# Optimization experiments

Hardware: AMD Instinct MI355X
Metric: run time of the kernel (lower is better)

The kernel has to match this reference:

```python
import jax, jax.numpy as jnp
import numpy as np

T_STEPS, BATCH, DX, DH = 128, 128, 1024, 1024
N_GATES = 5


def setup_inputs() -> dict:
    key = jax.random.key(0)
    ks = jax.random.split(key, 4)
    scale_x = 1.0 / np.sqrt(DX)
    scale_h = 1.0 / np.sqrt(DH)
    inputs = jax.random.normal(ks[0], (T_STEPS, BATCH, DX), dtype=jnp.float32)
    memories = jax.random.normal(ks[1], (T_STEPS, BATCH, DH), dtype=jnp.float32)
    h0 = jnp.zeros((BATCH, DH), dtype=jnp.float32)
    c0 = jnp.zeros((BATCH, DH), dtype=jnp.float32)
    Wx = jax.random.normal(ks[2], (N_GATES * DH, DX), dtype=jnp.float32) * scale_x
    bx = jnp.zeros((N_GATES * DH,), dtype=jnp.float32)
    Wh = jax.random.normal(ks[3], (N_GATES * DH, DH), dtype=jnp.float32) * scale_h
    # forget-gate bias (second chunk) initialized to 1, as in reset_parameters_
    bh = jnp.zeros((N_GATES * DH,), dtype=jnp.float32).at[DH:2 * DH].set(1.0)
    return {"inputs": inputs, "memories": memories, "h0": h0, "c0": c0,
            "Wx": Wx, "bx": bx, "Wh": Wh, "bh": bh}


def reference(inputs, memories, h0, c0, Wx, bx, Wh, bh):
    # EpLSTMCell.loop: time-major scan of the custom gated cell.
    # Gate order: I, F, G, O, R (tied forget gate: it = 1 - ft).
    def step(carry, inp):
        h, c = carry
        xt, mt = inp
        gx = jnp.dot(xt, Wx.T) + bx      # [B, 5*Dh]
        gh = jnp.dot(h, Wh.T) + bh       # [B, 5*Dh]
        Xi, Xf, Xg, Xo, Xr = jnp.split(gx, N_GATES, axis=-1)
        Hi, Hf, Hg, Ho, Hr = jnp.split(gh, N_GATES, axis=-1)
        ft = jax.nn.sigmoid(Xf + Hf)
        ot = jax.nn.sigmoid(Xo + Ho)
        it = 1.0 - ft                    # tied forget gate
        gt = jnp.tanh(Xg + Hg)
        rt = jax.nn.sigmoid(Xr + Hr)     # episodic memory gate
        ct = ft * c + it * gt + rt * jnp.tanh(mt)
        ht = ot * jnp.tanh(ct)
        return (ht, ct), ht

    (_, _), outs = jax.lax.scan(step, (h0, c0), (inputs, memories))
    return outs  # [T, B, Dh]
```

## Files before the change

### kernel.cpp

```cpp
#include <hip/hip_runtime.h>

#define T_STEPS 128
#define BATCH   128
#define DX      1024
#define DH      1024
#define BDH     (BATCH * DH)
#define BDX     (BATCH * DX)
#define PLW     40

typedef __attribute__((ext_vector_type(8)))  short short8;
typedef __attribute__((ext_vector_type(16))) float f32x16;
typedef __attribute__((ext_vector_type(4)))  float f32x4v;
typedef __attribute__((ext_vector_type(2)))  float f32x2;
typedef __attribute__((ext_vector_type(4)))  unsigned u32x4;
typedef __attribute__((ext_vector_type(2)))  _Float16 f16x2;

static __device__ __forceinline__ unsigned short f2bf(float f) {
    union { float f; unsigned u; } v; v.f = f;
    unsigned r = v.u + 0x7fffu + ((v.u >> 16) & 1u);
    return (unsigned short)(r >> 16);
}
static __device__ __forceinline__ short8 pack_bf16x8(f32x4v lo, f32x4v hi) {
    union { unsigned short u[8]; short8 v; } pk;
    pk.u[0]=f2bf(lo[0]); pk.u[1]=f2bf(lo[1]); pk.u[2]=f2bf(lo[2]); pk.u[3]=f2bf(lo[3]);
    pk.u[4]=f2bf(hi[0]); pk.u[5]=f2bf(hi[1]); pk.u[6]=f2bf(hi[2]); pk.u[7]=f2bf(hi[3]);
    return pk.v;
}
static __device__ __forceinline__ float sigf(float x) {
    float u = __expf(-fabsf(x));
    float b = 1.0f / (1.0f + u);
    return x >= 0.0f ? b : 1.0f - b;
}
static __device__ __forceinline__ float tanhfast(float x) {
    float u = __expf(-2.0f * fabsf(x));
    float r = (1.0f - u) / (1.0f + u);
    return x >= 0.0f ? r : -r;
}


__global__ __launch_bounds__(256) void prep_x(const float* __restrict__ x,
                                              unsigned short* __restrict__ Xb) {
    const size_t i8 = ((size_t)blockIdx.x * 256 + threadIdx.x) * 8;
    f32x4v lo = __builtin_nontemporal_load((const f32x4v*)(x + i8));
    f32x4v hi = __builtin_nontemporal_load((const f32x4v*)(x + i8 + 4));
    short8 v = pack_bf16x8(lo, hi);
    __builtin_nontemporal_store(v, (short8*)(Xb + i8));
}

__global__ __launch_bounds__(256) void prep_tm(const float* __restrict__ mem,
                                               _Float16* __restrict__ TM) {
    const size_t i8 = ((size_t)blockIdx.x * 256 + threadIdx.x) * 8;
    f32x4v lo = __builtin_nontemporal_load((const f32x4v*)(mem + i8));
    f32x4v hi = __builtin_nontemporal_load((const f32x4v*)(mem + i8 + 4));
    union { _Float16 h[8]; u32x4 q; } V;
    #pragma unroll
    for (int j = 0; j < 4; ++j) V.h[j]     = (_Float16)tanhfast(lo[j]);
    #pragma unroll
    for (int j = 0; j < 4; ++j) V.h[4 + j] = (_Float16)tanhfast(hi[j]);
    __builtin_nontemporal_store(V.q, (u32x4*)(TM + i8));
}

__global__ __launch_bounds__(256) void init_seed(const float* __restrict__ h0,
                                                 unsigned short* __restrict__ hseq,
                                                 unsigned* __restrict__ gflag) {
    const int i = blockIdx.x * 256 + threadIdx.x;
    if (i < BDH) hseq[i] = f2bf(h0[i]);
    if (blockIdx.x < 2) gflag[blockIdx.x * 256 + threadIdx.x] = 0;
}

__global__ __launch_bounds__(128) void prep_wxp(const float* __restrict__ Wx,
                                                const float* __restrict__ bx,
                                                const float* __restrict__ bh,
                                                unsigned short* __restrict__ Wxp,
                                                float* __restrict__ bp) {
    const int p = blockIdx.x;
    const int js = p >> 5, g = (p >> 3) & 3, jj = p & 7;
    const int srow = (g + 1) * 1024 + js * 8 + jj;
    const int k = threadIdx.x * 8;
    f32x4v lo = __builtin_nontemporal_load((const f32x4v*)(Wx + (size_t)srow * DX + k));
    f32x4v hi = __builtin_nontemporal_load((const f32x4v*)(Wx + (size_t)srow * DX + k + 4));
    short8 v = pack_bf16x8(lo, hi);
    __builtin_nontemporal_store(v, (short8*)(Wxp + (size_t)p * 1024 + k));
    if (threadIdx.x == 0) bp[p] = bx[srow] + bh[srow];
}

template<bool XBF16>
__global__ __launch_bounds__(256, 2) void gx_prepass3(
    const void* __restrict__ xsrc, const unsigned short* __restrict__ Wxp,
    const float* __restrict__ bp, _Float16* __restrict__ Gx)
{
    extern __shared__ char sm[];
    _Float16* pl16 = (_Float16*)(sm + 65536);

    const int bid = blockIdx.x;
    const int c  = bid & 7;
    const int js = bid >> 3;
    const int tid = threadIdx.x;

    {
        const int row = tid >> 3;
        const int koff = (tid & 7) * 128;
        const int sw = (row & 7) << 4;
        const unsigned short* src = Wxp + (size_t)(js * 32 + row) * 1024 + koff;
        char* dst = sm + row * 2048;
        #pragma unroll
        for (int it = 0; it < 16; ++it) {
            short8 v = __builtin_nontemporal_load((const short8*)(src + it * 8));
            *(short8*)(dst + (((koff + it * 8) * 2) ^ sw)) = v;
        }
    }

    const int rrow = tid >> 1;
    const int jjb  = (tid & 1) * 4;
    float bias_f[16];
    #pragma unroll
    for (int q = 0; q < 4; ++q)
        #pragma unroll
        for (int g = 0; g < 4; ++g)
            bias_f[q * 4 + g] = bp[js * 32 + g * 8 + (jjb + q)];

    const int wave = tid >> 6, lane = tid & 63;
    const int k8 = (lane >> 5) * 8;
    const char* wrow = sm + (lane & 31) * 2048;
    const int sw2 = ((lane & 31) & 7) << 4;
    __syncthreads();

    for (int i = 0; i < 16; ++i) {
        const int mt = c * 16 + i;
        const int arow = mt * 128 + wave * 32 + (lane & 31);
        f32x16 a0 = {}, a1 = {};

        if (XBF16) {
            const unsigned short* xp = (const unsigned short*)xsrc + (size_t)arow * 1024 + k8;
            #pragma unroll 8
            for (int ks = 0; ks < 64; ++ks) {
                short8 a = *(const short8*)(xp + ks * 16);
                short8 b = *(const short8*)(wrow + ((ks * 32 + k8 * 2) ^ sw2));
                if (ks & 1) a1 = __builtin_amdgcn_mfma_f32_32x32x16_bf16(a, b, a1, 0, 0, 0);
                else        a0 = __builtin_amdgcn_mfma_f32_32x32x16_bf16(a, b, a0, 0, 0, 0);
            }
        } else {
            const float* Af = (const float*)xsrc + (size_t)arow * 1024 + k8;
            #pragma unroll 8
            for (int ks = 0; ks < 64; ++ks) {
                f32x4v lo = *(const f32x4v*)(Af + ks * 16);
                f32x4v hi = *(const f32x4v*)(Af + ks * 16 + 4);
                union { unsigned u32[4]; short8 v; } pk;
                pk.u32[0] = __builtin_amdgcn_perm(__float_as_uint(lo[1]), __float_as_uint(lo[0]), 0x07060302u);
                pk.u32[1] = __builtin_amdgcn_perm(__float_as_uint(lo[3]), __float_as_uint(lo[2]), 0x07060302u);
                pk.u32[2] = __builtin_amdgcn_perm(__float_as_uint(hi[1]), __float_as_uint(hi[0]), 0x07060302u);
                pk.u32[3] = __builtin_amdgcn_perm(__float_as_uint(hi[3]), __float_as_uint(hi[2]), 0x07060302u);
                short8 b = *(const short8*)(wrow + ((ks * 32 + k8 * 2) ^ sw2));
                if (ks & 1) a1 = __builtin_amdgcn_mfma_f32_32x32x16_bf16(pk.v, b, a1, 0, 0, 0);
                else        a0 = __builtin_amdgcn_mfma_f32_32x32x16_bf16(pk.v, b, a0, 0, 0, 0);
            }
        }
        f32x16 r = a0 + a1;

        #pragma unroll
        for (int ii = 0; ii < 16; ++ii) {
            const int rowc = (ii & 3) + 8 * (ii >> 2) + 4 * (lane >> 5);
            pl16[(wave * 32 + rowc) * 40 + (lane & 31)] = (_Float16)r[ii];
        }
        __syncthreads();

        {
            union { _Float16 h[16]; u32x4 q[2]; } V;
            #pragma unroll
            for (int q = 0; q < 4; ++q)
                #pragma unroll
                for (int g = 0; g < 4; ++g)
                    V.h[q * 4 + g] = (_Float16)(
                        (float)pl16[rrow * 40 + g * 8 + (jjb + q)] + bias_f[q * 4 + g]);
            _Float16* dst = Gx + ((size_t)(mt * 128 + rrow) * 4096 + js * 32 + jjb * 4);
            __builtin_nontemporal_store(V.q[0], (u32x4*)dst);
            __builtin_nontemporal_store(V.q[1], (u32x4*)(dst + 8));
        }
        __syncthreads();
    }
}

template<bool USE_TM>
__global__ __launch_bounds__(256, 1) void eplstm_h(
    const _Float16* __restrict__ Gx,  const void* __restrict__ tmv,
    const float* __restrict__ Wh,     const float* __restrict__ c0,
    unsigned short* __restrict__ hseq, float* __restrict__ out,
    unsigned* __restrict__ gflag)
{
    __shared__ float pl[4 * 32 * PLW];

    const int bid = blockIdx.x;
    const int js  = (bid >> 3) * 4 + (bid & 3);
    const int bhh = (bid >> 2) & 1;
    const int tid = threadIdx.x;

    const int wave = tid >> 6, lane = tid & 63;
    const int mh = wave >> 1, kh = wave & 1;
    const int arow = bhh * 64 + mh * 32 + (lane & 31);
    const int k8 = (lane >> 5) * 8;
    const int p = lane & 31;
    const int word = (p & 7) * 4 + (p >> 3);
    float* plw = pl + wave * 32 * PLW;
    unsigned long long* fb = (unsigned long long*)(gflag + bhh * 128);

    short8 breg[32];
    {
        const int r = lane & 31;
        const int g = r >> 3, jj = r & 7;
        const float* Wrow = Wh + (size_t)((g + 1) * 1024 + js * 8 + jj) * 1024
                          + kh * 512 + k8;
        #pragma unroll
        for (int ks = 0; ks < 32; ++ks) {
            f32x4v lo = *(const f32x4v*)(Wrow + ks * 16);
            f32x4v hi = *(const f32x4v*)(Wrow + ks * 16 + 4);
            breg[ks] = pack_bf16x8(lo, hi);
        }
    }

    const int e0 = tid * 2;
    const int row_e = e0 >> 3;
    const int jj0 = e0 & 7;
    const int brow = bhh * 64 + row_e;
    const size_t obase = (size_t)brow * DH + js * 8 + jj0;
    const int mh_e = row_e >> 5, r_e = row_e & 31;
    float2 creg = *(const float2*)(c0 + obase);

    for (int t = 0; t < T_STEPS; ++t) {
        u32x4 gxv = __builtin_nontemporal_load(
            (const u32x4*)(Gx + ((size_t)(t * BATCH + brow) * 4096 + js * 32 + jj0 * 4)));
        f16x2 tm2 = {};
        f32x2 mv = {};
        if (USE_TM) {
            tm2 = __builtin_nontemporal_load(
                (const f16x2*)((const _Float16*)tmv + (size_t)t * BDH + obase));
        } else {
            mv = __builtin_nontemporal_load(
                (const f32x2*)((const float*)tmv + (size_t)t * BDH + obase));
        }

        if (t > 0) {
            if (wave == 0) {
                for (;;) {
                    unsigned long long fv = __hip_atomic_load(
                        &fb[lane], __ATOMIC_RELAXED, __HIP_MEMORY_SCOPE_AGENT);
                    if (__all(((unsigned)fv >= (unsigned)t) &&
                              ((unsigned)(fv >> 32) >= (unsigned)t))) break;
                    __builtin_amdgcn_s_sleep(2);
                }
            }
            __syncthreads();
        }

        const unsigned short* hp = hseq + (size_t)t * BDH + (size_t)arow * DH + kh * 512 + k8;
        f32x16 a0 = {}, a1 = {};
        #pragma unroll
        for (int ks = 0; ks < 32; ++ks) {
            short8 a = *(const short8*)(hp + ks * 16);
            if (ks & 1) a1 = __builtin_amdgcn_mfma_f32_32x32x16_bf16(a, breg[ks], a1, 0, 0, 0);
            else        a0 = __builtin_amdgcn_mfma_f32_32x32x16_bf16(a, breg[ks], a0, 0, 0, 0);
        }
        f32x16 r = a0 + a1;
        #pragma unroll
        for (int ii = 0; ii < 16; ++ii) {
            const int rowc = (ii & 3) + 8 * (ii >> 2) + 4 * (lane >> 5);
            plw[rowc * PLW + word] = r[ii];
        }
        __syncthreads();

        float4 p0A = *(const float4*)(pl + ((((mh_e << 1) | 0) * 32 + r_e) * PLW + (jj0 + 0) * 4));
        float4 p0B = *(const float4*)(pl + ((((mh_e << 1) | 1) * 32 + r_e) * PLW + (jj0 + 0) * 4));
        float4 p1A = *(const float4*)(pl + ((((mh_e << 1) | 0) * 32 + r_e) * PLW + (jj0 + 1) * 4));
        float4 p1B = *(const float4*)(pl + ((((mh_e << 1) | 1) * 32 + r_e) * PLW + (jj0 + 1) * 4));
        union { u32x4 u; _Float16 h[8]; } G; G.u = gxv;

        float hv[2];
        {
            const float gF = (float)G.h[0] + p0A.x + p0B.x;
            const float gG = (float)G.h[1] + p0A.y + p0B.y;
            const float gO = (float)G.h[2] + p0A.z + p0B.z;
            const float gR = (float)G.h[3] + p0A.w + p0B.w;
            const float ft = sigf(gF), ot = sigf(gO), rt = sigf(gR);
            const float gt = tanhfast(gG);
            const float tmv0 = USE_TM ? (float)tm2[0] : tanhfast(mv[0]);
            const float cv = ft * creg.x + (1.f - ft) * gt + rt * tmv0;
            creg.x = cv;
            hv[0] = ot * tanhfast(cv);
        }
        {
            const float gF = (float)G.h[4] + p1A.x + p1B.x;
            const float gG = (float)G.h[5] + p1A.y + p1B.y;
            const float gO = (float)G.h[6] + p1A.z + p1B.z;
            const float gR = (float)G.h[7] + p1A.w + p1B.w;
            const float ft = sigf(gF), ot = sigf(gO), rt = sigf(gR);
            const float gt = tanhfast(gG);
            const float tmv1 = USE_TM ? (float)tm2[1] : tanhfast(mv[1]);
            const float cv = ft * creg.y + (1.f - ft) * gt + rt * tmv1;
            creg.y = cv;
            hv[1] = ot * tanhfast(cv);
        }
        const unsigned hp2 = (unsigned)f2bf(hv[0]) | ((unsigned)f2bf(hv[1]) << 16);
        __hip_atomic_store((unsigned*)(hseq + (size_t)(t + 1) * BDH + obase), hp2,
                           __ATOMIC_RELAXED, __HIP_MEMORY_SCOPE_AGENT);
        asm volatile("s_waitcnt vmcnt(0)" ::: "memory");
        __syncthreads();
        if (tid == 0 && t < T_STEPS - 1) {
            __hip_atomic_store(&gflag[bhh * 128 + js], (unsigned)(t + 1),
                               __ATOMIC_RELAXED, __HIP_MEMORY_SCOPE_AGENT);
        }
        f32x2 hvv = { hv[0], hv[1] };
        __builtin_nontemporal_store(hvv, (f32x2*)(out + (size_t)t * BDH + obase));
    }
}

template<bool XBF16>
__global__ __launch_bounds__(256, 1) void eplstm_persistent(
    const void*  __restrict__ xsrc, const float* __restrict__ mem,
    const float* __restrict__ Wx,   const float* __restrict__ Wh,
    const float* __restrict__ bxp,  const float* __restrict__ bhp,
    const float* __restrict__ c0,
    unsigned short* __restrict__ hseq, float* __restrict__ out,
    unsigned* __restrict__ bar)
{
    extern __shared__ char smem[];
    float* pl = reinterpret_cast<float*>(smem + 131072);

    const int bid = blockIdx.x;
    const int js  = bid >> 1;
    const int bhh = bid & 1;
    const int tid = threadIdx.x;

    {
        const int prow = tid >> 3;
        const int g = prow >> 3, jj = prow & 7;
        const int srow = (g + 1) * 1024 + js * 8 + jj;
        const int kc = (tid & 7) * 256;
        const int sw = (prow & 7) << 4;
        for (int it = 0; it < 32; ++it) {
            const int k = kc + it * 8;
            const float* src = (k < DX) ? (Wx + (size_t)srow * DX + k)
                                        : (Wh + (size_t)srow * DH + (k - DX));
            f32x4v lo = *(const f32x4v*)(src);
            f32x4v hi = *(const f32x4v*)(src + 4);
            short8 v = pack_bf16x8(lo, hi);
            *reinterpret_cast<short8*>(smem + prow * 4096 + ((k * 2) ^ sw)) = v;
        }
    }

    const int e0   = tid * 2;
    const int bl   = e0 >> 3;
    const int jj0  = e0 & 7;
    const int brow_g = bhh * 64 + bl;
    const size_t oidx = (size_t)brow_g * DH + js * 8 + jj0;
    float biasv[2][4];
    #pragma unroll
    for (int e2 = 0; e2 < 2; ++e2)
        #pragma unroll
        for (int g = 0; g < 4; ++g) {
            const int srow = (g + 1) * 1024 + js * 8 + jj0 + e2;
            biasv[e2][g] = bxp[srow] + bhp[srow];
        }
    float2 creg = *reinterpret_cast<const float2*>(c0 + oidx);
    const int mh_e = bl >> 5, rr = bl & 31;

    const int wave = tid >> 6;
    const int lane = tid & 63;
    const int mh = wave >> 1, kh = wave & 1;
    const int arow   = bhh * 64 + mh * 32 + (lane & 31);
    const int k8     = (lane >> 5) * 8;
    const int brow   = lane & 31;
    const char* bbase = smem + brow * 4096;
    const int swz    = (brow & 7) << 4;
    const int kbyte0 = kh * 2048 + k8 * 2;

    __syncthreads();

    for (int t = 0; t < T_STEPS; ++t) {
        f32x16 ac0 = {}, ac1 = {}, ac2 = {}, ac3 = {};
        if (XBF16 || kh == 1) {
            const unsigned short* Ab = kh
                ? (hseq + (size_t)t * BDH + (size_t)arow * DH + k8)
                : ((const unsigned short*)xsrc + (size_t)t * BDX + (size_t)arow * DX + k8);
            #pragma unroll 8
            for (int ks = 0; ks < 64; ++ks) {
                short8 a = *reinterpret_cast<const short8*>(Ab + ks * 16);
                short8 b = *reinterpret_cast<const short8*>(bbase + ((kbyte0 + ks * 32) ^ swz));
                if      ((ks & 3) == 0) ac0 = __builtin_amdgcn_mfma_f32_32x32x16_bf16(a, b, ac0, 0, 0, 0);
                else if ((ks & 3) == 1) ac1 = __builtin_amdgcn_mfma_f32_32x32x16_bf16(a, b, ac1, 0, 0, 0);
                else if ((ks & 3) == 2) ac2 = __builtin_amdgcn_mfma_f32_32x32x16_bf16(a, b, ac2, 0, 0, 0);
                else                    ac3 = __builtin_amdgcn_mfma_f32_32x32x16_bf16(a, b, ac3, 0, 0, 0);
            }
        } else {
            const float* Af = (const float*)xsrc + (size_t)t * BDX + (size_t)arow * DX + k8;
            #pragma unroll 4
            for (int ks = 0; ks < 64; ++ks) {
                f32x4v lo = *(const f32x4v*)(Af + ks * 16);
                f32x4v hi = *(const f32x4v*)(Af + ks * 16 + 4);
                short8 a = pack_bf16x8(lo, hi);
                short8 b = *reinterpret_cast<const short8*>(bbase + ((kbyte0 + ks * 32) ^ swz));
                if      ((ks & 3) == 0) ac0 = __builtin_amdgcn_mfma_f32_32x32x16_bf16(a, b, ac0, 0, 0, 0);
                else if ((ks & 3) == 1) ac1 = __builtin_amdgcn_mfma_f32_32x32x16_bf16(a, b, ac1, 0, 0, 0);
                else if ((ks & 3) == 2) ac2 = __builtin_amdgcn_mfma_f32_32x32x16_bf16(a, b, ac2, 0, 0, 0);
                else                    ac3 = __builtin_amdgcn_mfma_f32_32x32x16_bf16(a, b, ac3, 0, 0, 0);
            }
        }
        f32x16 r = (ac0 + ac1) + (ac2 + ac3);

        #pragma unroll
        for (int i = 0; i < 16; ++i) {
            const int row = (i & 3) + 8 * (i >> 2) + 4 * (lane >> 5);
            pl[(wave * 32 + row) * 33 + brow] = r[i];
        }
        __syncthreads();

        const float2 mt2 = *reinterpret_cast<const float2*>(mem + (size_t)t * BDH + oidx);
        float hv[2];
        #pragma unroll
        for (int e2 = 0; e2 < 2; ++e2) {
            const int jj = jj0 + e2;
            float gs[4];
            #pragma unroll
            for (int g = 0; g < 4; ++g) {
                const int col = g * 8 + jj;
                gs[g] = pl[((mh_e * 2 + 0) * 32 + rr) * 33 + col]
                      + pl[((mh_e * 2 + 1) * 32 + rr) * 33 + col]
                      + biasv[e2][g];
            }
            const float ft = 1.f / (1.f + expf(-gs[0]));
            const float gt = tanhf(gs[1]);
            const float ot = 1.f / (1.f + expf(-gs[2]));
            const float rt = 1.f / (1.f + expf(-gs[3]));
            const float cin = e2 ? creg.y : creg.x;
            const float mvv = e2 ? mt2.y : mt2.x;
            const float cv = ft * cin + (1.f - ft) * gt + rt * tanhf(mvv);
            if (e2) creg.y = cv; else creg.x = cv;
            hv[e2] = ot * tanhf(cv);
        }
        *reinterpret_cast<float2*>(out + (size_t)t * BDH + oidx) = make_float2(hv[0], hv[1]);
        const unsigned hpk = (unsigned)f2bf(hv[0]) | ((unsigned)f2bf(hv[1]) << 16);
        __hip_atomic_store((unsigned*)(hseq + (size_t)(t + 1) * BDH + oidx), hpk,
                           __ATOMIC_RELAXED, __HIP_MEMORY_SCOPE_AGENT);

        __syncthreads();
        if (t < T_STEPS - 1) {
            if (tid == 0) {
                const unsigned want = (unsigned)(t + 1);
                const unsigned arrived = __hip_atomic_fetch_add(
                    &bar[bhh * 32], 1u, __ATOMIC_RELAXED, __HIP_MEMORY_SCOPE_AGENT);
                if (arrived == want * 128u - 1u) {
                    __hip_atomic_store(&bar[64 + bhh * 32], want,
                                       __ATOMIC_RELAXED, __HIP_MEMORY_SCOPE_AGENT);
                } else {
                    while (__hip_atomic_load(&bar[64 + bhh * 32],
                                             __ATOMIC_RELAXED, __HIP_MEMORY_SCOPE_AGENT) < want)
                        __builtin_amdgcn_s_sleep(2);
                }
            }
            __syncthreads();
        }
    }
}

extern "C" void kernel_launch(void* const* d_in, const int* in_sizes, int n_in,
                              void* d_out, int out_size, void* d_ws, size_t ws_size,
                              hipStream_t stream) {
    const float* inputs   = (const float*)d_in[0];
    const float* memories = (const float*)d_in[1];
    const float* h0       = (const float*)d_in[2];
    const float* c0       = (const float*)d_in[3];
    const float* Wx       = (const float*)d_in[4];
    const float* bx       = (const float*)d_in[5];
    const float* Wh       = (const float*)d_in[6];
    const float* bh_      = (const float*)d_in[7];
    float* outp = (float*)d_out;

    char* ws = (char*)d_ws;
    size_t off = 0;
    auto alloc = [&](size_t bytes) {
        char* p = ws + off;
        off = (off + bytes + 255) & ~(size_t)255;
        return p;
    };
    unsigned*       gflag = (unsigned*)alloc(512 * sizeof(unsigned));
    unsigned short* hseq  = (unsigned short*)alloc((size_t)(T_STEPS + 1) * BDH * 2);

    const size_t wxp_b  = (size_t)4096 * 1024 * 2;
    const size_t bp_b   = 4096 * 4;
    const size_t gx_b   = (size_t)16384 * 4096 * 2;
    const size_t xb_b   = (size_t)T_STEPS * BDX * 2;
    const size_t tm_b   = (size_t)T_STEPS * BDH * 2;
    const size_t need_base = off + wxp_b + 256 + bp_b + 256 + gx_b + 256;
    const size_t need_xb   = need_base + xb_b + 256;
    const size_t need_tm   = need_xb + tm_b + 256;

    if (ws_size >= need_base) {
        unsigned short* Wxp = (unsigned short*)alloc(wxp_b);
        float*          bp  = (float*)alloc(bp_b);
        _Float16*       Gx  = (_Float16*)alloc(gx_b);
        const bool use_xb = (ws_size >= need_xb);
        unsigned short* Xb = use_xb ? (unsigned short*)alloc(xb_b) : nullptr;
        const bool use_tm = (ws_size >= need_tm);
        _Float16* TM = use_tm ? (_Float16*)alloc(tm_b) : nullptr;

        init_seed<<<512, 256, 0, stream>>>(h0, hseq, gflag);
        prep_wxp<<<4096, 128, 0, stream>>>(Wx, bx, bh_, Wxp, bp);
        if (use_tm) prep_tm<<<8192, 256, 0, stream>>>(memories, TM);

        const unsigned pre_smem = 65536 + 128 * 40 * 2;
        if (use_xb) {
            prep_x<<<8192, 256, 0, stream>>>(inputs, Xb);
            (void)hipFuncSetAttribute((const void*)gx_prepass3<true>,
                                      hipFuncAttributeMaxDynamicSharedMemorySize, pre_smem);
            gx_prepass3<true><<<1024, 256, pre_smem, stream>>>((const void*)Xb, Wxp, bp, Gx);
        } else {
            (void)hipFuncSetAttribute((const void*)gx_prepass3<false>,
                                      hipFuncAttributeMaxDynamicSharedMemorySize, pre_smem);
            gx_prepass3<false><<<1024, 256, pre_smem, stream>>>((const void*)inputs, Wxp, bp, Gx);
        }

        const void* tmv = use_tm ? (const void*)TM : (const void*)memories;
        if (use_tm) {
            void* kargs[] = { (void*)&Gx, (void*)&tmv, (void*)&Wh, (void*)&c0,
                              (void*)&hseq, (void*)&outp, (void*)&gflag };
            hipError_t err = hipLaunchCooperativeKernel((const void*)eplstm_h<true>,
                                                        dim3(256), dim3(256), kargs, 0, stream);
            if (err != hipSuccess)
                eplstm_h<true><<<256, 256, 0, stream>>>(Gx, tmv, Wh, c0, hseq, outp, gflag);
        } else {
            void* kargs[] = { (void*)&Gx, (void*)&tmv, (void*)&Wh, (void*)&c0,
                              (void*)&hseq, (void*)&outp, (void*)&gflag };
            hipError_t err = hipLaunchCooperativeKernel((const void*)eplstm_h<false>,
                                                        dim3(256), dim3(256), kargs, 0, stream);
            if (err != hipSuccess)
                eplstm_h<false><<<256, 256, 0, stream>>>(Gx, tmv, Wh, c0, hseq, outp, gflag);
        }
    } else {
        const bool use_xb = (ws_size >= off + xb_b + 256);
        unsigned short* Xb = use_xb ? (unsigned short*)alloc(xb_b) : nullptr;

        init_seed<<<512, 256, 0, stream>>>(h0, hseq, gflag);
        if (use_xb) prep_x<<<8192, 256, 0, stream>>>(inputs, Xb);

        const unsigned smem_bytes = 131072 + 9216 + 9216 + 64;
        const void* xsrc = use_xb ? (const void*)Xb : (const void*)inputs;
        if (use_xb) {
            (void)hipFuncSetAttribute((const void*)eplstm_persistent<true>,
                                      hipFuncAttributeMaxDynamicSharedMemorySize, smem_bytes);
            void* kargs[] = { (void*)&xsrc, (void*)&memories, (void*)&Wx, (void*)&Wh,
                              (void*)&bx, (void*)&bh_, (void*)&c0, (void*)&hseq,
                              (void*)&outp, (void*)&gflag };
            hipError_t err = hipLaunchCooperativeKernel(
                (const void*)eplstm_persistent<true>, dim3(256), dim3(256),
                kargs, smem_bytes, stream);
            if (err != hipSuccess) {
                eplstm_persistent<true><<<256, 256, smem_bytes, stream>>>(
                    xsrc, memories, Wx, Wh, bx, bh_, c0, hseq, outp, gflag);
            }
        } else {
            (void)hipFuncSetAttribute((const void*)eplstm_persistent<false>,
                                      hipFuncAttributeMaxDynamicSharedMemorySize, smem_bytes);
            void* kargs[] = { (void*)&xsrc, (void*)&memories, (void*)&Wx, (void*)&Wh,
                              (void*)&bx, (void*)&bh_, (void*)&c0, (void*)&hseq,
                              (void*)&outp, (void*)&gflag };
            hipError_t err = hipLaunchCooperativeKernel(
                (const void*)eplstm_persistent<false>, dim3(256), dim3(256),
                kargs, smem_bytes, stream);
            if (err != hipSuccess) {
                eplstm_persistent<false><<<256, 256, smem_bytes, stream>>>(
                    xsrc, memories, Wx, Wh, bx, bh_, c0, hseq, outp, gflag);
            }
        }
    }
}
```

Baseline: 1.625 ms.

## Fuse input projection into persistent recurrent kernel, computing it two steps ahead

Drops the separate Gx prepass kernel and the large fp16 Gx buffer. The recurrent cooperative kernel now keeps a bf16 slice of Wx in LDS and computes the input-gate MFMA for step t+2 after finishing step t, double-buffered in shared memory. The aim is to hide the x projection under the latency-bound serial recurrence and avoid writing and re-reading the Gx tensor. In exchange it adds per-step MFMA work and LDS pressure to the critical-path kernel, which could lengthen each step.

```diff
diff --git a/kernel.cpp b/kernel.cpp
--- a/kernel.cpp
+++ b/kernel.cpp
@@ -68,126 +68,20 @@
     if (blockIdx.x < 2) gflag[blockIdx.x * 256 + threadIdx.x] = 0;
 }
 
-__global__ __launch_bounds__(128) void prep_wxp(const float* __restrict__ Wx,
-                                                const float* __restrict__ bx,
-                                                const float* __restrict__ bh,
-                                                unsigned short* __restrict__ Wxp,
-                                                float* __restrict__ bp) {
-    const int p = blockIdx.x;
-    const int js = p >> 5, g = (p >> 3) & 3, jj = p & 7;
-    const int srow = (g + 1) * 1024 + js * 8 + jj;
-    const int k = threadIdx.x * 8;
-    f32x4v lo = __builtin_nontemporal_load((const f32x4v*)(Wx + (size_t)srow * DX + k));
-    f32x4v hi = __builtin_nontemporal_load((const f32x4v*)(Wx + (size_t)srow * DX + k + 4));
-    short8 v = pack_bf16x8(lo, hi);
-    __builtin_nontemporal_store(v, (short8*)(Wxp + (size_t)p * 1024 + k));
-    if (threadIdx.x == 0) bp[p] = bx[srow] + bh[srow];
-}
-
-template<bool XBF16>
-__global__ __launch_bounds__(256, 2) void gx_prepass3(
-    const void* __restrict__ xsrc, const unsigned short* __restrict__ Wxp,
-    const float* __restrict__ bp, _Float16* __restrict__ Gx)
-{
-    extern __shared__ char sm[];
-    _Float16* pl16 = (_Float16*)(sm + 65536);
-
-    const int bid = blockIdx.x;
-    const int c  = bid & 7;
-    const int js = bid >> 3;
-    const int tid = threadIdx.x;
-
-    {
-        const int row = tid >> 3;
-        const int koff = (tid & 7) * 128;
-        const int sw = (row & 7) << 4;
-        const unsigned short* src = Wxp + (size_t)(js * 32 + row) * 1024 + koff;
-        char* dst = sm + row * 2048;
-        #pragma unroll
-        for (int it = 0; it < 16; ++it) {
-            short8 v = __builtin_nontemporal_load((const short8*)(src + it * 8));
-            *(short8*)(dst + (((koff + it * 8) * 2) ^ sw)) = v;
-        }
-    }
-
-    const int rrow = tid >> 1;
-    const int jjb  = (tid & 1) * 4;
-    float bias_f[16];
-    #pragma unroll
-    for (int q = 0; q < 4; ++q)
-        #pragma unroll
-        for (int g = 0; g < 4; ++g)
-            bias_f[q * 4 + g] = bp[js * 32 + g * 8 + (jjb + q)];
-
-    const int wave = tid >> 6, lane = tid & 63;
-    const int k8 = (lane >> 5) * 8;
-    const char* wrow = sm + (lane & 31) * 2048;
-    const int sw2 = ((lane & 31) & 7) << 4;
-    __syncthreads();
-
-    for (int i = 0; i < 16; ++i) {
-        const int mt = c * 16 + i;
-        const int arow = mt * 128 + wave * 32 + (lane & 31);
-        f32x16 a0 = {}, a1 = {};
-
-        if (XBF16) {
-            const unsigned short* xp = (const unsigned short*)xsrc + (size_t)arow * 1024 + k8;
-            #pragma unroll 8
-            for (int ks = 0; ks < 64; ++ks) {
-                short8 a = *(const short8*)(xp + ks * 16);
-                short8 b = *(const short8*)(wrow + ((ks * 32 + k8 * 2) ^ sw2));
-                if (ks & 1) a1 = __builtin_amdgcn_mfma_f32_32x32x16_bf16(a, b, a1, 0, 0, 0);
-                else        a0 = __builtin_amdgcn_mfma_f32_32x32x16_bf16(a, b, a0, 0, 0, 0);
-            }
-        } else {
-            const float* Af = (const float*)xsrc + (size_t)arow * 1024 + k8;
-            #pragma unroll 8
-            for (int ks = 0; ks < 64; ++ks) {
-                f32x4v lo = *(const f32x4v*)(Af + ks * 16);
-                f32x4v hi = *(const f32x4v*)(Af + ks * 16 + 4);
-                union { unsigned u32[4]; short8 v; } pk;
-                pk.u32[0] = __builtin_amdgcn_perm(__float_as_uint(lo[1]), __float_as_uint(lo[0]), 0x07060302u);
-                pk.u32[1] = __builtin_amdgcn_perm(__float_as_uint(lo[3]), __float_as_uint(lo[2]), 0x07060302u);
-                pk.u32[2] = __builtin_amdgcn_perm(__float_as_uint(hi[1]), __float_as_uint(hi[0]), 0x07060302u);
-                pk.u32[3] = __builtin_amdgcn_perm(__float_as_uint(hi[3]), __float_as_uint(hi[2]), 0x07060302u);
-                short8 b = *(const short8*)(wrow + ((ks * 32 + k8 * 2) ^ sw2));
-                if (ks & 1) a1 = __builtin_amdgcn_mfma_f32_32x32x16_bf16(pk.v, b, a1, 0, 0, 0);
-                else        a0 = __builtin_amdgcn_mfma_f32_32x32x16_bf16(pk.v, b, a0, 0, 0, 0);
-            }
-        }
-        f32x16 r = a0 + a1;
-
-        #pragma unroll
-        for (int ii = 0; ii < 16; ++ii) {
-            const int rowc = (ii & 3) + 8 * (ii >> 2) + 4 * (lane >> 5);
-            pl16[(wave * 32 + rowc) * 40 + (lane & 31)] = (_Float16)r[ii];
-        }
-        __syncthreads();
-
-        {
-            union { _Float16 h[16]; u32x4 q[2]; } V;
-            #pragma unroll
-            for (int q = 0; q < 4; ++q)
-                #pragma unroll
-                for (int g = 0; g < 4; ++g)
-                    V.h[q * 4 + g] = (_Float16)(
-                        (float)pl16[rrow * 40 + g * 8 + (jjb + q)] + bias_f[q * 4 + g]);
-            _Float16* dst = Gx + ((size_t)(mt * 128 + rrow) * 4096 + js * 32 + jjb * 4);
-            __builtin_nontemporal_store(V.q[0], (u32x4*)dst);
-            __builtin_nontemporal_store(V.q[1], (u32x4*)(dst + 8));
-        }
-        __syncthreads();
-    }
-}
-
-template<bool USE_TM>
-__global__ __launch_bounds__(256, 1) void eplstm_h(
-    const _Float16* __restrict__ Gx,  const void* __restrict__ tmv,
-    const float* __restrict__ Wh,     const float* __restrict__ c0,
+__global__ __launch_bounds__(256, 1) void eplstm_f(
+    const unsigned short* __restrict__ Xb,
+    const _Float16* __restrict__ TM,
+    const float* __restrict__ Wx,
+    const float* __restrict__ Wh,
+    const float* __restrict__ bx,  const float* __restrict__ bh,
+    const float* __restrict__ c0,
     unsigned short* __restrict__ hseq, float* __restrict__ out,
     unsigned* __restrict__ gflag)
 {
-    __shared__ float pl[4 * 32 * PLW];
+    extern __shared__ char smem[];
+    float* pl   = (float*)(smem + 65536);
+    float* pl2a = (float*)(smem + 65536 + 20480);
+    float* pl2b = (float*)(smem + 65536 + 40960);
 
     const int bid = blockIdx.x;
     const int js  = (bid >> 3) * 4 + (bid & 3);
@@ -200,8 +94,27 @@
     const int k8 = (lane >> 5) * 8;
     const int p = lane & 31;
     const int word = (p & 7) * 4 + (p >> 3);
-    float* plw = pl + wave * 32 * PLW;
+    float* plw   = pl   + wave * 32 * PLW;
+    float* pl2aw = pl2a + wave * 32 * PLW;
+    float* pl2bw = pl2b + wave * 32 * PLW;
     unsigned long long* fb = (unsigned long long*)(gflag + bhh * 128);
+
+    {
+        const int row = tid >> 3;
+        const int g = row >> 3, jj = row & 7;
+        const int srow = (g + 1) * 1024 + js * 8 + jj;
+        const int sw = (row & 7) << 4;
+        const float* W = Wx + (size_t)srow * 1024;
+        char* dst = smem + row * 2048;
+        #pragma unroll
+        for (int it = 0; it < 16; ++it) {
+            const int k = (tid & 7) * 128 + it * 8;
+            f32x4v lo = __builtin_nontemporal_load((const f32x4v*)(W + k));
+            f32x4v hi = __builtin_nontemporal_load((const f32x4v*)(W + k + 4));
+            short8 v = pack_bf16x8(lo, hi);
+            *(short8*)(dst + ((k * 2) ^ sw)) = v;
+        }
+    }
 
     short8 breg[32];
     {
@@ -223,20 +136,47 @@
     const int brow = bhh * 64 + row_e;
     const size_t obase = (size_t)brow * DH + js * 8 + jj0;
     const int mh_e = row_e >> 5, r_e = row_e & 31;
+    float biasv[2][4];
+    #pragma unroll
+    for (int e2 = 0; e2 < 2; ++e2)
+        #pragma unroll
+        for (int g = 0; g < 4; ++g) {
+            const int srow = (g + 1) * 1024 + js * 8 + jj0 + e2;
+            biasv[e2][g] = bx[srow] + bh[srow];
+        }
     float2 creg = *(const float2*)(c0 + obase);
 
+    const char* wrow = smem + (lane & 31) * 2048;
+    const int sw2 = ((lane & 31) & 7) << 4;
+    const int kbyte0 = (kh * 512 + k8) * 2;
+
+    auto x_round = [&](int tt, float* slot) {
+        const unsigned short* xp = Xb + (size_t)tt * BDX + (size_t)arow * DX
+                                 + kh * 512 + k8;
+        f32x16 xa0 = {}, xa1 = {};
+        #pragma unroll 8
+        for (int ks = 0; ks < 32; ++ks) {
+            short8 a = *(const short8*)(xp + ks * 16);
+            short8 b = *(const short8*)(wrow + ((kbyte0 + ks * 32) ^ sw2));
+            if (ks & 1) xa1 = __builtin_amdgcn_mfma_f32_32x32x16_bf16(a, b, xa1, 0, 0, 0);
+            else        xa0 = __builtin_amdgcn_mfma_f32_32x32x16_bf16(a, b, xa0, 0, 0, 0);
+        }
+        f32x16 xr = xa0 + xa1;
+        #pragma unroll
+        for (int ii = 0; ii < 16; ++ii) {
+            const int rowc = (ii & 3) + 8 * (ii >> 2) + 4 * (lane >> 5);
+            slot[rowc * PLW + word] = xr[ii];
+        }
+    };
+
+    __syncthreads();
+
+    x_round(0, pl2aw);
+    x_round(1, pl2bw);
+
     for (int t = 0; t < T_STEPS; ++t) {
-        u32x4 gxv = __builtin_nontemporal_load(
-            (const u32x4*)(Gx + ((size_t)(t * BATCH + brow) * 4096 + js * 32 + jj0 * 4)));
-        f16x2 tm2 = {};
-        f32x2 mv = {};
-        if (USE_TM) {
-            tm2 = __builtin_nontemporal_load(
-                (const f16x2*)((const _Float16*)tmv + (size_t)t * BDH + obase));
-        } else {
-            mv = __builtin_nontemporal_load(
-                (const f32x2*)((const float*)tmv + (size_t)t * BDH + obase));
-        }
+        f16x2 tm2 = __builtin_nontemporal_load(
+            (const f16x2*)(TM + (size_t)t * BDH + obase));
 
         if (t > 0) {
             if (wave == 0) {
@@ -267,34 +207,36 @@
         }
         __syncthreads();
 
-        float4 p0A = *(const float4*)(pl + ((((mh_e << 1) | 0) * 32 + r_e) * PLW + (jj0 + 0) * 4));
-        float4 p0B = *(const float4*)(pl + ((((mh_e << 1) | 1) * 32 + r_e) * PLW + (jj0 + 0) * 4));
-        float4 p1A = *(const float4*)(pl + ((((mh_e << 1) | 0) * 32 + r_e) * PLW + (jj0 + 1) * 4));
-        float4 p1B = *(const float4*)(pl + ((((mh_e << 1) | 1) * 32 + r_e) * PLW + (jj0 + 1) * 4));
-        union { u32x4 u; _Float16 h[8]; } G; G.u = gxv;
+        const float* px = (t & 1) ? pl2b : pl2a;
+        float4 h0A = *(const float4*)(pl + ((((mh_e << 1) | 0) * 32 + r_e) * PLW + (jj0 + 0) * 4));
+        float4 h0B = *(const float4*)(pl + ((((mh_e << 1) | 1) * 32 + r_e) * PLW + (jj0 + 0) * 4));
+        float4 h1A = *(const float4*)(pl + ((((mh_e << 1) | 0) * 32 + r_e) * PLW + (jj0 + 1) * 4));
+        float4 h1B = *(const float4*)(pl + ((((mh_e << 1) | 1) * 32 + r_e) * PLW + (jj0 + 1) * 4));
+        float4 x0A = *(const float4*)(px + ((((mh_e << 1) | 0) * 32 + r_e) * PLW + (jj0 + 0) * 4));
+        float4 x0B = *(const float4*)(px + ((((mh_e << 1) | 1) * 32 + r_e) * PLW + (jj0 + 0) * 4));
+        float4 x1A = *(const float4*)(px + ((((mh_e << 1) | 0) * 32 + r_e) * PLW + (jj0 + 1) * 4));
+        float4 x1B = *(const float4*)(px + ((((mh_e << 1) | 1) * 32 + r_e) * PLW + (jj0 + 1) * 4));
 
         float hv[2];
         {
-            const float gF = (float)G.h[0] + p0A.x + p0B.x;
-            const float gG = (float)G.h[1] + p0A.y + p0B.y;
-            const float gO = (float)G.h[2] + p0A.z + p0B.z;
-            const float gR = (float)G.h[3] + p0A.w + p0B.w;
+            const float gF = biasv[0][0] + h0A.x + h0B.x + x0A.x + x0B.x;
+            const float gG = biasv[0][1] + h0A.y + h0B.y + x0A.y + x0B.y;
+            const float gO = biasv[0][2] + h0A.z + h0B.z + x0A.z + x0B.z;
+            const float gR = biasv[0][3] + h0A.w + h0B.w + x0A.w + x0B.w;
             const float ft = sigf(gF), ot = sigf(gO), rt = sigf(gR);
             const float gt = tanhfast(gG);
-            const float tmv0 = USE_TM ? (float)tm2[0] : tanhfast(mv[0]);
-            const float cv = ft * creg.x + (1.f - ft) * gt + rt * tmv0;
+            const float cv = ft * creg.x + (1.f - ft) * gt + rt * (float)tm2[0];
             creg.x = cv;
             hv[0] = ot * tanhfast(cv);
         }
         {
-            const float gF = (float)G.h[4] + p1A.x + p1B.x;
-            const float gG = (float)G.h[5] + p1A.y + p1B.y;
-            const float gO = (float)G.h[6] + p1A.z + p1B.z;
-            const float gR = (float)G.h[7] + p1A.w + p1B.w;
+            const float gF = biasv[1][0] + h1A.x + h1B.x + x1A.x + x1B.x;
+            const float gG = biasv[1][1] + h1A.y + h1B.y + x1A.y + x1B.y;
+            const float gO = biasv[1][2] + h1A.z + h1B.z + x1A.z + x1B.z;
+            const float gR = biasv[1][3] + h1A.w + h1B.w + x1A.w + x1B.w;
             const float ft = sigf(gF), ot = sigf(gO), rt = sigf(gR);
             const float gt = tanhfast(gG);
-            const float tmv1 = USE_TM ? (float)tm2[1] : tanhfast(mv[1]);
-            const float cv = ft * creg.y + (1.f - ft) * gt + rt * tmv1;
+            const float cv = ft * creg.y + (1.f - ft) * gt + rt * (float)tm2[1];
             creg.y = cv;
             hv[1] = ot * tanhfast(cv);
         }
@@ -309,6 +251,8 @@
         }
         f32x2 hvv = { hv[0], hv[1] };
         __builtin_nontemporal_store(hvv, (f32x2*)(out + (size_t)t * BDH + obase));
+
+        if (t + 2 < T_STEPS) x_round(t + 2, (t & 1) ? pl2bw : pl2aw);
     }
 }
 
@@ -483,55 +427,29 @@
     unsigned*       gflag = (unsigned*)alloc(512 * sizeof(unsigned));
     unsigned short* hseq  = (unsigned short*)alloc((size_t)(T_STEPS + 1) * BDH * 2);
 
-    const size_t wxp_b  = (size_t)4096 * 1024 * 2;
-    const size_t bp_b   = 4096 * 4;
-    const size_t gx_b   = (size_t)16384 * 4096 * 2;
-    const size_t xb_b   = (size_t)T_STEPS * BDX * 2;
-    const size_t tm_b   = (size_t)T_STEPS * BDH * 2;
-    const size_t need_base = off + wxp_b + 256 + bp_b + 256 + gx_b + 256;
-    const size_t need_xb   = need_base + xb_b + 256;
-    const size_t need_tm   = need_xb + tm_b + 256;
-
-    if (ws_size >= need_base) {
-        unsigned short* Wxp = (unsigned short*)alloc(wxp_b);
-        float*          bp  = (float*)alloc(bp_b);
-        _Float16*       Gx  = (_Float16*)alloc(gx_b);
-        const bool use_xb = (ws_size >= need_xb);
-        unsigned short* Xb = use_xb ? (unsigned short*)alloc(xb_b) : nullptr;
-        const bool use_tm = (ws_size >= need_tm);
-        _Float16* TM = use_tm ? (_Float16*)alloc(tm_b) : nullptr;
+    const size_t xb_b = (size_t)T_STEPS * BDX * 2;
+    const size_t tm_b = (size_t)T_STEPS * BDH * 2;
+    const size_t need_b = off + xb_b + 256 + tm_b + 256;
+
+    if (ws_size >= need_b) {
+        unsigned short* Xb = (unsigned short*)alloc(xb_b);
+        _Float16*       TM = (_Float16*)alloc(tm_b);
 
         init_seed<<<512, 256, 0, stream>>>(h0, hseq, gflag);
-        prep_wxp<<<4096, 128, 0, stream>>>(Wx, bx, bh_, Wxp, bp);
-        if (use_tm) prep_tm<<<8192, 256, 0, stream>>>(memories, TM);
-
-        const unsigned pre_smem = 65536 + 128 * 40 * 2;
-        if (use_xb) {
-            prep_x<<<8192, 256, 0, stream>>>(inputs, Xb);
-            (void)hipFuncSetAttribute((const void*)gx_prepass3<true>,
-                                      hipFuncAttributeMaxDynamicSharedMemorySize, pre_smem);
-            gx_prepass3<true><<<1024, 256, pre_smem, stream>>>((const void*)Xb, Wxp, bp, Gx);
-        } else {
-            (void)hipFuncSetAttribute((const void*)gx_prepass3<false>,
-                                      hipFuncAttributeMaxDynamicSharedMemorySize, pre_smem);
-            gx_prepass3<false><<<1024, 256, pre_smem, stream>>>((const void*)inputs, Wxp, bp, Gx);
-        }
-
-        const void* tmv = use_tm ? (const void*)TM : (const void*)memories;
-        if (use_tm) {
-            void* kargs[] = { (void*)&Gx, (void*)&tmv, (void*)&Wh, (void*)&c0,
-                              (void*)&hseq, (void*)&outp, (void*)&gflag };
-            hipError_t err = hipLaunchCooperativeKernel((const void*)eplstm_h<true>,
-                                                        dim3(256), dim3(256), kargs, 0, stream);
-            if (err != hipSuccess)
-                eplstm_h<true><<<256, 256, 0, stream>>>(Gx, tmv, Wh, c0, hseq, outp, gflag);
-        } else {
-            void* kargs[] = { (void*)&Gx, (void*)&tmv, (void*)&Wh, (void*)&c0,
-                              (void*)&hseq, (void*)&outp, (void*)&gflag };
-            hipError_t err = hipLaunchCooperativeKernel((const void*)eplstm_h<false>,
-                                                        dim3(256), dim3(256), kargs, 0, stream);
-            if (err != hipSuccess)
-                eplstm_h<false><<<256, 256, 0, stream>>>(Gx, tmv, Wh, c0, hseq, outp, gflag);
+        prep_x<<<8192, 256, 0, stream>>>(inputs, Xb);
+        prep_tm<<<8192, 256, 0, stream>>>(memories, TM);
+
+        const unsigned smem_bytes = 65536 + 3 * 4 * 32 * PLW * 4;
+        (void)hipFuncSetAttribute((const void*)eplstm_f,
+                                  hipFuncAttributeMaxDynamicSharedMemorySize, smem_bytes);
+        void* kargs[] = { (void*)&Xb, (void*)&TM, (void*)&Wx, (void*)&Wh,
+                          (void*)&bx, (void*)&bh_, (void*)&c0, (void*)&hseq,
+                          (void*)&outp, (void*)&gflag };
+        hipError_t err = hipLaunchCooperativeKernel((const void*)eplstm_f, dim3(256),
+                                                    dim3(256), kargs, smem_bytes, stream);
+        if (err != hipSuccess) {
+            eplstm_f<<<256, 256, smem_bytes, stream>>>(Xb, TM, Wx, Wh, bx, bh_,
+                                                       c0, hseq, outp, gflag);
         }
     } else {
         const bool use_xb = (ws_size >= off + xb_b + 256);
```

Result: no change. 1.641 ms (+0.9%).
